# Kernel tuning notes

Measured on AMD Instinct MI355X. Metric: run time of the kernel, lower is better.

The kernel has to match this reference:

```python
import jax, jax.numpy as jnp
import numpy as np

B, N, D = 4, 1024, 512
H, Dv, Dq = 8, 64, 64
NUM_BUCKETS = 64
LN_EPS = 1e-5


def setup_inputs() -> dict:
    key = jax.random.key(0)
    ks = jax.random.split(key, 10)
    x = jax.random.normal(ks[0], (B, N, D), dtype=jnp.float32)
    ts = jnp.sort(jax.random.randint(ks[1], (B, N), 0, 1_000_000), axis=1).astype(jnp.int64)
    cm = jnp.triu(jnp.ones((N, N), dtype=bool), k=1)  # causal: mask j > i
    pm = jnp.zeros((B, N), dtype=bool)                # no padding
    uvqk = 0.02 * jax.random.normal(ks[2], (D, 2 * H * Dv + 2 * H * Dq), dtype=jnp.float32)
    lim = float(np.sqrt(6.0 / (H * Dv + D)))
    o_w = jax.random.uniform(ks[3], (H * Dv, D), minval=-lim, maxval=lim, dtype=jnp.float32)
    o_b = jnp.zeros((D,), dtype=jnp.float32)
    ln_x_w = jnp.ones((D,), jnp.float32); ln_x_b = jnp.zeros((D,), jnp.float32)
    ln_a_w = jnp.ones((H * Dv,), jnp.float32); ln_a_b = jnp.zeros((H * Dv,), jnp.float32)
    ts_w = 0.02 * jax.random.normal(ks[4], (NUM_BUCKETS + 1,), dtype=jnp.float32)
    pos_w = 0.02 * jax.random.normal(ks[5], (2 * N - 1,), dtype=jnp.float32)
    return {"x": x, "ts": ts, "cm": cm, "pm": pm, "uvqk": uvqk, "o_w": o_w, "o_b": o_b,
            "ln_x_w": ln_x_w, "ln_x_b": ln_x_b, "ln_a_w": ln_a_w, "ln_a_b": ln_a_b,
            "ts_w": ts_w, "pos_w": pos_w}


def _layernorm(x, w, b):
    m = jnp.mean(x, axis=-1, keepdims=True)
    v = jnp.mean(jnp.square(x - m), axis=-1, keepdims=True)
    return (x - m) / jnp.sqrt(v + LN_EPS) * w + b


def _rel_bias(ts, ts_w, pos_w):
    # positional part: pb[i, j] = pos_w[j - i + N - 1], shape [N, N]
    idx = jnp.arange(N)
    pb = pos_w[idx[None, :] - idx[:, None] + N - 1]
    # bucketed time part
    ext = jnp.concatenate([ts, ts[:, N - 1:N]], axis=1)           # [B, N+1]
    diff = ext[:, 1:, None] - ext[:, None, :-1]                   # [B, N, N]
    logd = jnp.log(jnp.maximum(jnp.abs(diff), 1).astype(jnp.float32))
    bk = jnp.clip((logd / 0.301).astype(jnp.int32), 0, NUM_BUCKETS)
    return pb[None] + ts_w[bk]                                    # [B, N, N]


def reference(x, ts, cm, pm, uvqk, o_w, o_b, ln_x_w, ln_x_b, ln_a_w, ln_a_b, ts_w, pos_w):
    nx = _layernorm(x, ln_x_w, ln_x_b)                            # [B, N, D]
    out = jax.nn.silu(jnp.einsum('bnd,de->bne', nx, uvqk))        # [B, N, 2HDv+2HDq]
    u, v, q, k = jnp.split(out, [H * Dv, 2 * H * Dv, 2 * H * Dv + H * Dq], axis=-1)
    q = q.reshape(B, N, H, Dq)
    k = k.reshape(B, N, H, Dq)
    v = v.reshape(B, N, H, Dv)
    qk = jnp.einsum('bihd,bjhd->bhij', q, k) + _rel_bias(ts, ts_w, pos_w)[:, None]
    qk = jax.nn.silu(qk) / N
    qk = jnp.where(cm[None, None], 0.0, qk)          # causal mask
    qk = jnp.where(pm[:, None, None, :], 0.0, qk)    # padding mask on keys
    ao = jnp.einsum('bhij,bjhd->bihd', qk, v).reshape(B, N, H * Dv)
    ao = _layernorm(ao, ln_a_w, ln_a_b)
    u = u.reshape(B, N, H * Dv)
    y = (u * ao) @ o_w + o_b + x
    return jnp.where(pm[:, :, None], 0.0, y)
```

## Files before the change

kernel.cpp:

```cpp
#include <hip/hip_runtime.h>
#include <hip/hip_bf16.h>


typedef __attribute__((ext_vector_type(8))) short short8;
typedef __attribute__((ext_vector_type(4))) short bf4;
typedef __attribute__((ext_vector_type(4))) float floatx4;

#define MFMA_BF16 __builtin_amdgcn_mfma_f32_16x16x32_bf16

static __device__ __forceinline__ short f2bf(float f) {
  unsigned u = __builtin_bit_cast(unsigned, f);
  u = (u + 0x7fffu + ((u >> 16) & 1u)) >> 16;
  return (short)u;
}
static __device__ __forceinline__ unsigned pk_bf16(float a, float b) {
  __hip_bfloat162 h = __float22bfloat162_rn(float2{a, b});
  unsigned u;
  __builtin_memcpy(&u, &h, 4);
  return u;
}
static __device__ __forceinline__ short lo16(unsigned u) { return (short)(u & 0xffffu); }
static __device__ __forceinline__ short hi16(unsigned u) { return (short)(u >> 16); }
static __device__ __forceinline__ float bf2f(short s) {
  unsigned u = ((unsigned)(unsigned short)s) << 16;
  return __builtin_bit_cast(float, u);
}
static __device__ __forceinline__ float silu_f(float x) {
  return x / (1.f + __expf(-x));
}
static __device__ __forceinline__ void gl_lds16(const void* g, void* l) {
  __builtin_amdgcn_global_load_lds(
      (const __attribute__((address_space(1))) unsigned int*)g,
      (__attribute__((address_space(3))) unsigned int*)l, 16, 0, 0);
}

__global__ __launch_bounds__(256) void prep_kernel(
    const float* __restrict__ x, const int* __restrict__ ts,
    const float* __restrict__ uvqk, const float* __restrict__ o_w,
    const float* __restrict__ ln_x_w, const float* __restrict__ ln_x_b,
    const float* __restrict__ ts_w, const float* __restrict__ pos_w,
    short* __restrict__ nx, short* __restrict__ uvqk_t,
    short* __restrict__ o_wt, short* __restrict__ bias) {
  __shared__ float tile[32][33];
  const int id = blockIdx.x;
  const int t = threadIdx.x;
  if (id < 4096) {
    const int b = id >> 10, i = id & 1023;
    int ie = i + 1; if (ie > 1023) ie = 1023;
    const int tse = ts[(b << 10) + ie];
    const int j0 = t * 4;
    int4 tj = *(const int4*)&ts[(b << 10) + j0];
    const int* tjp = (const int*)&tj;
    float ov[4];
#pragma unroll
    for (int e = 0; e < 4; ++e) {
      int dt = tse - tjp[e];
      float ad = fabsf((float)dt);
      if (ad < 1.f) ad = 1.f;
      int bkt = (int)(__logf(ad) * (1.f / 0.301f));
      if (bkt > 64) bkt = 64;
      ov[e] = pos_w[j0 + e - i + 1023] + ts_w[bkt];
    }
    uint2 o2 = {pk_bf16(ov[0], ov[1]), pk_bf16(ov[2], ov[3])};
    *(uint2*)&bias[((size_t)id << 10) + j0] = o2;
  } else if (id < 5120) {
    const int lane = t & 63;
    const int row = ((id - 4096) << 2) + (t >> 6);
    const int c0 = lane * 8;
    const float* xr = x + (size_t)row * 512;
    float v[8];
    *(float4*)&v[0] = *(const float4*)(xr + c0);
    *(float4*)&v[4] = *(const float4*)(xr + c0 + 4);
    float s = 0.f, sq = 0.f;
#pragma unroll
    for (int e = 0; e < 8; ++e) { s += v[e]; sq += v[e] * v[e]; }
#pragma unroll
    for (int off = 32; off > 0; off >>= 1) {
      s += __shfl_xor(s, off);
      sq += __shfl_xor(sq, off);
    }
    float m = s * (1.f / 512.f);
    float var = sq * (1.f / 512.f) - m * m;
    float rinv = rsqrtf(var + 1e-5f);
    float wv[8], bv[8];
    *(float4*)&wv[0] = *(const float4*)(ln_x_w + c0);
    *(float4*)&wv[4] = *(const float4*)(ln_x_w + c0 + 4);
    *(float4*)&bv[0] = *(const float4*)(ln_x_b + c0);
    *(float4*)&bv[4] = *(const float4*)(ln_x_b + c0 + 4);
    float o[8];
#pragma unroll
    for (int e = 0; e < 8; ++e) o[e] = (v[e] - m) * rinv * wv[e] + bv[e];
    uint4 o4 = {pk_bf16(o[0], o[1]), pk_bf16(o[2], o[3]),
                pk_bf16(o[4], o[5]), pk_bf16(o[6], o[7])};
    *(uint4*)(nx + (size_t)row * 512 + c0) = o4;
  } else {
    const float* src; short* dst; int R, C, bc, br;
    if (id < 6144) {
      int idm = id - 5120;
      src = uvqk; dst = uvqk_t; R = 512; C = 2048;
      bc = (idm & 63) * 32; br = (idm >> 6) * 32;
    } else {
      int idm = id - 6144;
      src = o_w; dst = o_wt; R = 512; C = 512;
      bc = (idm & 15) * 32; br = (idm >> 4) * 32;
    }
    const int c = t & 31, r0 = t >> 5;
#pragma unroll
    for (int p = 0; p < 4; ++p) {
      int r = r0 + p * 8;
      tile[r][c] = src[(size_t)(br + r) * C + bc + c];
    }
    __syncthreads();
#pragma unroll
    for (int p = 0; p < 4; ++p) {
      int r = r0 + p * 8;
      dst[(size_t)(bc + r) * R + br + c] = f2bf(tile[c][r]);
    }
  }
}

__global__ __launch_bounds__(256) void gemm1_kernel(
    const short* __restrict__ A, const short* __restrict__ Bt,
    short* __restrict__ u_buf, short* __restrict__ vt_buf,
    short* __restrict__ q_buf, short* __restrict__ k_buf) {
  __shared__ __align__(16) short As[2][128 * 32];
  __shared__ __align__(16) short Bs[2][64 * 32];
  const int t = threadIdx.x;
  const int lane = t & 63, w = t >> 6;
  const int quad = lane >> 4, l15 = lane & 15;
  const int m0 = blockIdx.x * 128, n0 = blockIdx.y * 64;
  const int wm = (w & 1) * 64, wn = (w >> 1) * 32;
  const int lr = lane >> 2, lc = (lane & 3) * 8;
  floatx4 acc[4][2];
#pragma unroll
  for (int i = 0; i < 4; ++i)
#pragma unroll
    for (int j = 0; j < 2; ++j) acc[i][j] = (floatx4){0.f, 0.f, 0.f, 0.f};

  for (int k0 = 0; k0 < 512; k0 += 64) {
    __syncthreads();
#pragma unroll
    for (int c = 0; c < 2; ++c) {
#pragma unroll
      for (int p = 0; p < 2; ++p) {
        int ra = w * 32 + p * 16;
        gl_lds16(&A[(size_t)(m0 + ra + lr) * 512 + k0 + c * 32 + lc], &As[c][ra * 32]);
      }
      int rb = w * 16;
      gl_lds16(&Bt[(size_t)(n0 + rb + lr) * 512 + k0 + c * 32 + lc], &Bs[c][rb * 32]);
    }
    __syncthreads();
#pragma unroll
    for (int c = 0; c < 2; ++c) {
      short8 af[4], bfr[2];
#pragma unroll
      for (int mi = 0; mi < 4; ++mi) af[mi] = *(const short8*)&As[c][(wm + mi * 16 + l15) * 32 + quad * 8];
#pragma unroll
      for (int ni = 0; ni < 2; ++ni) bfr[ni] = *(const short8*)&Bs[c][(wn + ni * 16 + l15) * 32 + quad * 8];
#pragma unroll
      for (int mi = 0; mi < 4; ++mi)
#pragma unroll
        for (int ni = 0; ni < 2; ++ni)
          acc[mi][ni] = MFMA_BF16(af[mi], bfr[ni], acc[mi][ni], 0, 0, 0);
    }
  }
  const int seg = n0 >> 9, cbase = n0 & 511;
  if (seg == 0) {
#pragma unroll
    for (int mi = 0; mi < 4; ++mi)
#pragma unroll
      for (int ni = 0; ni < 2; ++ni) {
        int row0 = m0 + wm + mi * 16 + quad * 4;
        int c = cbase + wn + ni * 16 + l15;
        float v0 = silu_f(acc[mi][ni][0]), v1 = silu_f(acc[mi][ni][1]);
        float v2 = silu_f(acc[mi][ni][2]), v3 = silu_f(acc[mi][ni][3]);
        unsigned pa = pk_bf16(v0, v1), pb = pk_bf16(v2, v3);
        u_buf[(size_t)row0 * 512 + c] = lo16(pa);
        u_buf[(size_t)(row0 + 1) * 512 + c] = hi16(pa);
        u_buf[(size_t)(row0 + 2) * 512 + c] = lo16(pb);
        u_buf[(size_t)(row0 + 3) * 512 + c] = hi16(pb);
      }
  } else if (seg == 1) {
#pragma unroll
    for (int mi = 0; mi < 4; ++mi)
#pragma unroll
      for (int ni = 0; ni < 2; ++ni) {
        int c = cbase + wn + ni * 16 + l15;
        int h = c >> 6, d = c & 63;
        int row0 = m0 + wm + mi * 16 + quad * 4;
        int b_ = row0 >> 10, nb = row0 & 1023;
        float v0 = silu_f(acc[mi][ni][0]) * (1.f / 1024.f);
        float v1 = silu_f(acc[mi][ni][1]) * (1.f / 1024.f);
        float v2 = silu_f(acc[mi][ni][2]) * (1.f / 1024.f);
        float v3 = silu_f(acc[mi][ni][3]) * (1.f / 1024.f);
        uint2 sv = {pk_bf16(v0, v1), pk_bf16(v2, v3)};
        *(uint2*)&vt_buf[(((size_t)(b_ * 8 + h) * 64 + d) << 10) + nb] = sv;
      }
  } else {
    short* dst = (seg == 2) ? q_buf : k_buf;
#pragma unroll
    for (int mi = 0; mi < 4; ++mi)
#pragma unroll
      for (int ni = 0; ni < 2; ++ni) {
        int row0 = m0 + wm + mi * 16 + quad * 4;
        int c = cbase + wn + ni * 16 + l15;
        int b_ = row0 >> 10, nb = row0 & 1023;
        size_t base = ((((size_t)(b_ * 8 + (c >> 6))) << 10) + nb) * 64 + (c & 63);
        float v0 = silu_f(acc[mi][ni][0]), v1 = silu_f(acc[mi][ni][1]);
        float v2 = silu_f(acc[mi][ni][2]), v3 = silu_f(acc[mi][ni][3]);
        unsigned pa = pk_bf16(v0, v1), pb = pk_bf16(v2, v3);
        dst[base] = lo16(pa);
        dst[base + 64] = hi16(pa);
        dst[base + 128] = lo16(pb);
        dst[base + 192] = hi16(pb);
      }
  }
}

__global__ __launch_bounds__(256, 4) void attn_kernel(
    const short* __restrict__ q_buf, const short* __restrict__ k_buf,
    const short* __restrict__ vt_buf, const short* __restrict__ bias_buf,
    short* __restrict__ ao_part) {
  __shared__ __align__(16) short k_s[64][72];
  __shared__ __align__(16) short vt_s[64][72];
  __shared__ __align__(16) short p_s[64][72];

  const int t = threadIdx.x;
  const int lane = t & 63, w = t >> 6;
  const int quad = lane >> 4, l15 = lane & 15;
  const int bh = blockIdx.x, pair = blockIdx.y, jh = blockIdx.z;
  const int b = bh >> 3, h = bh & 7;
  const short* qh = q_buf + (size_t)bh * 65536;
  const short* kh = k_buf + (size_t)bh * 65536;
  const short* vth = vt_buf + (size_t)bh * 65536;
  const int sr = t >> 2, sc = (t & 3) * 16;
  const int it1 = 15 - pair;
  const int i0a = pair * 64, i0b = it1 * 64;

  const short* qra = &qh[(size_t)(i0a + w * 16 + l15) * 64 + quad * 8];
  const short* qrb = &qh[(size_t)(i0b + w * 16 + l15) * 64 + quad * 8];
  short8 aqa0 = *(const short8*)qra, aqa1 = *(const short8*)(qra + 32);
  short8 aqb0 = *(const short8*)qrb, aqb1 = *(const short8*)(qrb + 32);

  floatx4 aoa[4], aob[4];
#pragma unroll
  for (int ni = 0; ni < 4; ++ni) {
    aoa[ni] = (floatx4){0.f, 0.f, 0.f, 0.f};
    aob[ni] = (floatx4){0.f, 0.f, 0.f, 0.f};
  }

  float4 kr0, kr1, vr0, vr1;
  {
    int j0 = jh * 64;
    kr0 = *(const float4*)&kh[(size_t)(j0 + sr) * 64 + sc];
    kr1 = *(const float4*)&kh[(size_t)(j0 + sr) * 64 + sc + 8];
    vr0 = *(const float4*)&vth[(size_t)sr * 1024 + j0 + sc];
    vr1 = *(const float4*)&vth[(size_t)sr * 1024 + j0 + sc + 8];
  }

  for (int jt = jh; jt <= it1; jt += 4) {
    const int j0 = jt * 64;
    __syncthreads();
    *(float4*)&k_s[sr][sc] = kr0;
    *(float4*)&k_s[sr][sc + 8] = kr1;
    *(float4*)&vt_s[sr][sc] = vr0;
    *(float4*)&vt_s[sr][sc + 8] = vr1;
    {
      int jn = (jt + 4 <= it1) ? jt + 4 : jt;
      int jn0 = jn * 64;
      kr0 = *(const float4*)&kh[(size_t)(jn0 + sr) * 64 + sc];
      kr1 = *(const float4*)&kh[(size_t)(jn0 + sr) * 64 + sc + 8];
      vr0 = *(const float4*)&vth[(size_t)sr * 1024 + jn0 + sc];
      vr1 = *(const float4*)&vth[(size_t)sr * 1024 + jn0 + sc + 8];
    }
    __syncthreads();

#pragma unroll
    for (int unit = 0; unit < 2; ++unit) {
      if (unit == 1 && jt > pair) break;
      const int i0 = unit ? i0a : i0b;
      const bool diag = (jt == (unit ? pair : it1));
      const short8 aq0 = unit ? aqa0 : aqb0;
      const short8 aq1 = unit ? aqa1 : aqb1;
      floatx4* ao = unit ? aoa : aob;
      short br[4][4];
      {
        const short* bb = &bias_buf[((size_t)(b * 1024 + i0 + w * 16 + quad * 4) << 10) + j0 + l15];
#pragma unroll
        for (int ni = 0; ni < 4; ++ni)
#pragma unroll
          for (int r2 = 0; r2 < 4; ++r2)
            br[ni][r2] = bb[((size_t)r2 << 10) + ni * 16];
      }
      floatx4 s[4];
#pragma unroll
      for (int ni = 0; ni < 4; ++ni)
#pragma unroll
        for (int r2 = 0; r2 < 4; ++r2) s[ni][r2] = bf2f(br[ni][r2]);
#pragma unroll
      for (int ni = 0; ni < 4; ++ni) {
        s[ni] = MFMA_BF16(aq0, *(const short8*)&k_s[ni * 16 + l15][quad * 8], s[ni], 0, 0, 0);
        s[ni] = MFMA_BF16(aq1, *(const short8*)&k_s[ni * 16 + l15][32 + quad * 8], s[ni], 0, 0, 0);
      }
#pragma unroll
      for (int ni = 0; ni < 4; ++ni) {
        int j_loc = ni * 16 + l15;
        float pv[4];
#pragma unroll
        for (int r2 = 0; r2 < 4; ++r2) {
          int i_loc = w * 16 + quad * 4 + r2;
          float p = silu_f(s[ni][r2]);
          pv[r2] = (diag && j_loc > i_loc) ? 0.f : p;
        }
        unsigned pa = pk_bf16(pv[0], pv[1]), pb = pk_bf16(pv[2], pv[3]);
        int ib = w * 16 + quad * 4;
        p_s[ib][j_loc] = lo16(pa);
        p_s[ib + 1][j_loc] = hi16(pa);
        p_s[ib + 2][j_loc] = lo16(pb);
        p_s[ib + 3][j_loc] = hi16(pb);
      }
      short8 ap0 = *(const short8*)&p_s[w * 16 + l15][quad * 8];
      short8 ap1 = *(const short8*)&p_s[w * 16 + l15][32 + quad * 8];
#pragma unroll
      for (int ni = 0; ni < 4; ++ni) {
        ao[ni] = MFMA_BF16(ap0, *(const short8*)&vt_s[ni * 16 + l15][quad * 8], ao[ni], 0, 0, 0);
        ao[ni] = MFMA_BF16(ap1, *(const short8*)&vt_s[ni * 16 + l15][32 + quad * 8], ao[ni], 0, 0, 0);
      }
    }
  }
  short* aod = ao_part + (size_t)jh * 2097152;
#pragma unroll
  for (int half = 0; half < 2; ++half) {
    const int i0 = half ? i0b : i0a;
    floatx4* ao = half ? aob : aoa;
#pragma unroll
    for (int ni = 0; ni < 4; ++ni) {
      int gi0 = i0 + w * 16 + quad * 4;
      int d = ni * 16 + l15;
      unsigned pa = pk_bf16(ao[ni][0], ao[ni][1]);
      unsigned pb = pk_bf16(ao[ni][2], ao[ni][3]);
      size_t base = ((size_t)(b * 1024 + gi0)) * 512 + h * 64 + d;
      aod[base] = lo16(pa);
      aod[base + 512] = hi16(pa);
      aod[base + 1024] = lo16(pb);
      aod[base + 1536] = hi16(pb);
    }
  }
}

__global__ __launch_bounds__(256) void ln_mul_kernel(
    const short* __restrict__ ao_part, const short* __restrict__ u,
    const float* __restrict__ w_, const float* __restrict__ b_,
    short* __restrict__ g) {
  const int lane = threadIdx.x & 63;
  const int row = (blockIdx.x << 2) + (threadIdx.x >> 6);
  const int c0 = lane * 8;
  short8 a0 = *(const short8*)(ao_part + (size_t)row * 512 + c0);
  short8 a1 = *(const short8*)(ao_part + 2097152 + (size_t)row * 512 + c0);
  short8 a2 = *(const short8*)(ao_part + 4194304 + (size_t)row * 512 + c0);
  short8 a3 = *(const short8*)(ao_part + 6291456 + (size_t)row * 512 + c0);
  float v[8];
#pragma unroll
  for (int e = 0; e < 8; ++e)
    v[e] = (bf2f(a0[e]) + bf2f(a1[e])) + (bf2f(a2[e]) + bf2f(a3[e]));
  float s = 0.f, sq = 0.f;
#pragma unroll
  for (int e = 0; e < 8; ++e) { s += v[e]; sq += v[e] * v[e]; }
#pragma unroll
  for (int off = 32; off > 0; off >>= 1) {
    s += __shfl_xor(s, off);
    sq += __shfl_xor(sq, off);
  }
  float m = s * (1.f / 512.f);
  float var = sq * (1.f / 512.f) - m * m;
  float rinv = rsqrtf(var + 1e-5f);
  float wv[8], bv[8];
  *(float4*)&wv[0] = *(const float4*)(w_ + c0);
  *(float4*)&wv[4] = *(const float4*)(w_ + c0 + 4);
  *(float4*)&bv[0] = *(const float4*)(b_ + c0);
  *(float4*)&bv[4] = *(const float4*)(b_ + c0 + 4);
  short8 uv = *(const short8*)(u + (size_t)row * 512 + c0);
  float o[8];
#pragma unroll
  for (int e = 0; e < 8; ++e)
    o[e] = bf2f(uv[e]) * ((v[e] - m) * rinv * wv[e] + bv[e]);
  uint4 o4 = {pk_bf16(o[0], o[1]), pk_bf16(o[2], o[3]),
              pk_bf16(o[4], o[5]), pk_bf16(o[6], o[7])};
  *(uint4*)(g + (size_t)row * 512 + c0) = o4;
}

__global__ __launch_bounds__(256) void gemm2_kernel(
    const short* __restrict__ G, const short* __restrict__ Wt,
    const float* __restrict__ o_b, const float* __restrict__ x,
    float* __restrict__ out) {
  __shared__ __align__(16) short As[2][64 * 32];
  __shared__ __align__(16) short Bs[2][64 * 32];
  const int t = threadIdx.x;
  const int lane = t & 63, w = t >> 6;
  const int quad = lane >> 4, l15 = lane & 15;
  const int m0 = blockIdx.x * 64, n0 = blockIdx.y * 64;
  const int lr = lane >> 2, lc = (lane & 3) * 8;
  floatx4 acc[4];
#pragma unroll
  for (int j = 0; j < 4; ++j) acc[j] = (floatx4){0.f, 0.f, 0.f, 0.f};

  for (int k0 = 0; k0 < 512; k0 += 64) {
    __syncthreads();
#pragma unroll
    for (int c = 0; c < 2; ++c) {
      int ra = w * 16;
      gl_lds16(&G[(size_t)(m0 + ra + lr) * 512 + k0 + c * 32 + lc], &As[c][ra * 32]);
      gl_lds16(&Wt[(size_t)(n0 + ra + lr) * 512 + k0 + c * 32 + lc], &Bs[c][ra * 32]);
    }
    __syncthreads();
#pragma unroll
    for (int c = 0; c < 2; ++c) {
      short8 af = *(const short8*)&As[c][(w * 16 + l15) * 32 + quad * 8];
#pragma unroll
      for (int ni = 0; ni < 4; ++ni) {
        short8 bfr = *(const short8*)&Bs[c][(ni * 16 + l15) * 32 + quad * 8];
        acc[ni] = MFMA_BF16(af, bfr, acc[ni], 0, 0, 0);
      }
    }
  }
#pragma unroll
  for (int ni = 0; ni < 4; ++ni)
#pragma unroll
    for (int r = 0; r < 4; ++r) {
      int row = m0 + w * 16 + quad * 4 + r;
      int c = n0 + ni * 16 + l15;
      out[(size_t)row * 512 + c] = acc[ni][r] + o_b[c] + x[(size_t)row * 512 + c];
    }
}

extern "C" void kernel_launch(void* const* d_in, const int* in_sizes, int n_in,
                              void* d_out, int out_size, void* d_ws, size_t ws_size,
                              hipStream_t stream) {
  const float* x = (const float*)d_in[0];
  const int* ts = (const int*)d_in[1];
  const float* uvqk = (const float*)d_in[4];
  const float* o_w = (const float*)d_in[5];
  const float* o_b = (const float*)d_in[6];
  const float* ln_x_w = (const float*)d_in[7];
  const float* ln_x_b = (const float*)d_in[8];
  const float* ln_a_w = (const float*)d_in[9];
  const float* ln_a_b = (const float*)d_in[10];
  const float* ts_w = (const float*)d_in[11];
  const float* pos_w = (const float*)d_in[12];
  float* out = (float*)d_out;

  char* ws = (char*)d_ws;
  short* nx = (short*)(ws + 0);
  short* uvqk_t = (short*)(ws + 4194304);
  short* o_wt = (short*)(ws + 6291456);
  short* u_buf = (short*)(ws + 6815744);
  short* q_buf = (short*)(ws + 11010048);
  short* k_buf = (short*)(ws + 15204352);
  short* vt_buf = (short*)(ws + 19398656);
  short* bias_buf = (short*)(ws + 23592960);
  short* ao_part = (short*)(ws + 31981568);
  short* g_buf = nx;

  hipLaunchKernelGGL(prep_kernel, dim3(6400), dim3(256), 0, stream,
                     x, ts, uvqk, o_w, ln_x_w, ln_x_b, ts_w, pos_w,
                     nx, uvqk_t, o_wt, bias_buf);
  hipLaunchKernelGGL(gemm1_kernel, dim3(32, 32), dim3(256), 0, stream, nx, uvqk_t, u_buf, vt_buf, q_buf, k_buf);
  hipLaunchKernelGGL(attn_kernel, dim3(32, 8, 4), dim3(256), 0, stream, q_buf, k_buf, vt_buf, bias_buf, ao_part);
  hipLaunchKernelGGL(ln_mul_kernel, dim3(1024), dim3(256), 0, stream, ao_part, u_buf, ln_a_w, ln_a_b, g_buf);
  hipLaunchKernelGGL(gemm2_kernel, dim3(64, 8), dim3(256), 0, stream, g_buf, o_wt, o_b, x, out);
}
```

Measured before the change: 141.0 us.

## Fuse five pipeline kernels into one cooperative persistent kernel with grid syncs

Replaces the five separate launches (prep, gemm1, attention, layernorm-mul, gemm2) with a single cooperative kernel of 512 blocks that loops over work items per phase and separates phases with grid.sync(). The aim is to remove per-launch overhead and inter-kernel gaps. The cost is that each phase is now limited to 512 resident blocks processing 1024 sub-tiles, plus grid-wide barriers. Load balance in the causal attention phase may also suffer. The old multi-kernel path remains as a fallback if the cooperative launch fails.

```diff
diff --git a/kernel.cpp b/kernel.cpp
--- a/kernel.cpp
+++ b/kernel.cpp
@@ -1,9 +1,11 @@
 #include <hip/hip_runtime.h>
 #include <hip/hip_bf16.h>
+#include <hip/hip_cooperative_groups.h>
+
+namespace cg = cooperative_groups;
 
 
 typedef __attribute__((ext_vector_type(8))) short short8;
-typedef __attribute__((ext_vector_type(4))) short bf4;
 typedef __attribute__((ext_vector_type(4))) float floatx4;
 
 #define MFMA_BF16 __builtin_amdgcn_mfma_f32_16x16x32_bf16
@@ -32,6 +34,412 @@
   __builtin_amdgcn_global_load_lds(
       (const __attribute__((address_space(1))) unsigned int*)g,
       (__attribute__((address_space(3))) unsigned int*)l, 16, 0, 0);
+}
+
+__global__ __launch_bounds__(256, 2) void mega_kernel(
+    const float* __restrict__ x, const int* __restrict__ ts,
+    const float* __restrict__ uvqk, const float* __restrict__ o_w,
+    const float* __restrict__ o_b, const float* __restrict__ ln_x_w,
+    const float* __restrict__ ln_x_b, const float* __restrict__ ln_a_w,
+    const float* __restrict__ ln_a_b, const float* __restrict__ ts_w,
+    const float* __restrict__ pos_w,
+    short* __restrict__ nx, short* __restrict__ uvqk_t,
+    short* __restrict__ o_wt, short* __restrict__ u_buf,
+    short* __restrict__ q_buf, short* __restrict__ k_buf,
+    short* __restrict__ vt_buf, short* __restrict__ bias_buf,
+    short* __restrict__ ao_part, short* __restrict__ g_buf,
+    float* __restrict__ out) {
+  __shared__ __align__(16) char smem[27648];
+  cg::grid_group grid = cg::this_grid();
+
+  const int gid = blockIdx.x;
+  const int t = threadIdx.x;
+  const int lane = t & 63, w = t >> 6;
+  const int quad = lane >> 4, l15 = lane & 15;
+
+  for (int sub = gid; sub < 1024; sub += 512) {
+#pragma unroll
+    for (int r = 0; r < 4; ++r) {
+      const int id = sub * 4 + r;
+      const int b = id >> 10, i = id & 1023;
+      int ie = i + 1; if (ie > 1023) ie = 1023;
+      const int tse = ts[(b << 10) + ie];
+      const int j0 = t * 4;
+      int4 tj = *(const int4*)&ts[(b << 10) + j0];
+      const int* tjp = (const int*)&tj;
+      float ov[4];
+#pragma unroll
+      for (int e = 0; e < 4; ++e) {
+        int dt = tse - tjp[e];
+        float ad = fabsf((float)dt);
+        if (ad < 1.f) ad = 1.f;
+        int bkt = (int)(__logf(ad) * (1.f / 0.301f));
+        if (bkt > 64) bkt = 64;
+        ov[e] = pos_w[j0 + e - i + 1023] + ts_w[bkt];
+      }
+      uint2 o2 = {pk_bf16(ov[0], ov[1]), pk_bf16(ov[2], ov[3])};
+      *(uint2*)&bias_buf[((size_t)id << 10) + j0] = o2;
+    }
+    {
+      const int row = (sub << 2) + w;
+      const int c0 = lane * 8;
+      const float* xr = x + (size_t)row * 512;
+      float v[8];
+      *(float4*)&v[0] = *(const float4*)(xr + c0);
+      *(float4*)&v[4] = *(const float4*)(xr + c0 + 4);
+      float s = 0.f, sq = 0.f;
+#pragma unroll
+      for (int e = 0; e < 8; ++e) { s += v[e]; sq += v[e] * v[e]; }
+#pragma unroll
+      for (int off = 32; off > 0; off >>= 1) {
+        s += __shfl_xor(s, off);
+        sq += __shfl_xor(sq, off);
+      }
+      float m = s * (1.f / 512.f);
+      float var = sq * (1.f / 512.f) - m * m;
+      float rinv = rsqrtf(var + 1e-5f);
+      float wv[8], bv[8];
+      *(float4*)&wv[0] = *(const float4*)(ln_x_w + c0);
+      *(float4*)&wv[4] = *(const float4*)(ln_x_w + c0 + 4);
+      *(float4*)&bv[0] = *(const float4*)(ln_x_b + c0);
+      *(float4*)&bv[4] = *(const float4*)(ln_x_b + c0 + 4);
+      float o[8];
+#pragma unroll
+      for (int e = 0; e < 8; ++e) o[e] = (v[e] - m) * rinv * wv[e] + bv[e];
+      uint4 o4 = {pk_bf16(o[0], o[1]), pk_bf16(o[2], o[3]),
+                  pk_bf16(o[4], o[5]), pk_bf16(o[6], o[7])};
+      *(uint4*)(nx + (size_t)row * 512 + c0) = o4;
+    }
+    float (*tile)[33] = (float(*)[33])smem;
+    {
+      __syncthreads();
+      const int bc = (sub & 63) * 32, br = (sub >> 6) * 32;
+      const int c = t & 31, r0 = t >> 5;
+#pragma unroll
+      for (int p = 0; p < 4; ++p) {
+        int r = r0 + p * 8;
+        tile[r][c] = uvqk[(size_t)(br + r) * 2048 + bc + c];
+      }
+      __syncthreads();
+#pragma unroll
+      for (int p = 0; p < 4; ++p) {
+        int r = r0 + p * 8;
+        uvqk_t[(size_t)(bc + r) * 512 + br + c] = f2bf(tile[c][r]);
+      }
+    }
+    if (sub < 256) {
+      __syncthreads();
+      const int bc = (sub & 15) * 32, br = (sub >> 4) * 32;
+      const int c = t & 31, r0 = t >> 5;
+#pragma unroll
+      for (int p = 0; p < 4; ++p) {
+        int r = r0 + p * 8;
+        tile[r][c] = o_w[(size_t)(br + r) * 512 + bc + c];
+      }
+      __syncthreads();
+#pragma unroll
+      for (int p = 0; p < 4; ++p) {
+        int r = r0 + p * 8;
+        o_wt[(size_t)(bc + r) * 512 + br + c] = f2bf(tile[c][r]);
+      }
+    }
+  }
+  grid.sync();
+
+  for (int sub = gid; sub < 1024; sub += 512) {
+    short (*As)[128 * 32] = (short(*)[128 * 32])smem;
+    short (*Bs)[64 * 32] = (short(*)[64 * 32])(smem + 16384);
+    const int m0 = (sub & 31) * 128, n0 = (sub >> 5) * 64;
+    const int wm = (w & 1) * 64, wn = (w >> 1) * 32;
+    const int lr = lane >> 2, lc = (lane & 3) * 8;
+    floatx4 acc[4][2];
+#pragma unroll
+    for (int i = 0; i < 4; ++i)
+#pragma unroll
+      for (int j = 0; j < 2; ++j) acc[i][j] = (floatx4){0.f, 0.f, 0.f, 0.f};
+
+    for (int k0 = 0; k0 < 512; k0 += 64) {
+      __syncthreads();
+#pragma unroll
+      for (int c = 0; c < 2; ++c) {
+#pragma unroll
+        for (int p = 0; p < 2; ++p) {
+          int ra = w * 32 + p * 16;
+          gl_lds16(&nx[(size_t)(m0 + ra + lr) * 512 + k0 + c * 32 + lc], &As[c][ra * 32]);
+        }
+        int rb = w * 16;
+        gl_lds16(&uvqk_t[(size_t)(n0 + rb + lr) * 512 + k0 + c * 32 + lc], &Bs[c][rb * 32]);
+      }
+      __syncthreads();
+#pragma unroll
+      for (int c = 0; c < 2; ++c) {
+        short8 af[4], bfr[2];
+#pragma unroll
+        for (int mi = 0; mi < 4; ++mi) af[mi] = *(const short8*)&As[c][(wm + mi * 16 + l15) * 32 + quad * 8];
+#pragma unroll
+        for (int ni = 0; ni < 2; ++ni) bfr[ni] = *(const short8*)&Bs[c][(wn + ni * 16 + l15) * 32 + quad * 8];
+#pragma unroll
+        for (int mi = 0; mi < 4; ++mi)
+#pragma unroll
+          for (int ni = 0; ni < 2; ++ni)
+            acc[mi][ni] = MFMA_BF16(af[mi], bfr[ni], acc[mi][ni], 0, 0, 0);
+      }
+    }
+    const int seg = n0 >> 9, cbase = n0 & 511;
+    if (seg == 0) {
+#pragma unroll
+      for (int mi = 0; mi < 4; ++mi)
+#pragma unroll
+        for (int ni = 0; ni < 2; ++ni) {
+          int row0 = m0 + wm + mi * 16 + quad * 4;
+          int c = cbase + wn + ni * 16 + l15;
+          float v0 = silu_f(acc[mi][ni][0]), v1 = silu_f(acc[mi][ni][1]);
+          float v2 = silu_f(acc[mi][ni][2]), v3 = silu_f(acc[mi][ni][3]);
+          unsigned pa = pk_bf16(v0, v1), pb = pk_bf16(v2, v3);
+          u_buf[(size_t)row0 * 512 + c] = lo16(pa);
+          u_buf[(size_t)(row0 + 1) * 512 + c] = hi16(pa);
+          u_buf[(size_t)(row0 + 2) * 512 + c] = lo16(pb);
+          u_buf[(size_t)(row0 + 3) * 512 + c] = hi16(pb);
+        }
+    } else if (seg == 1) {
+#pragma unroll
+      for (int mi = 0; mi < 4; ++mi)
+#pragma unroll
+        for (int ni = 0; ni < 2; ++ni) {
+          int c = cbase + wn + ni * 16 + l15;
+          int h = c >> 6, d = c & 63;
+          int row0 = m0 + wm + mi * 16 + quad * 4;
+          int b_ = row0 >> 10, nb = row0 & 1023;
+          float v0 = silu_f(acc[mi][ni][0]) * (1.f / 1024.f);
+          float v1 = silu_f(acc[mi][ni][1]) * (1.f / 1024.f);
+          float v2 = silu_f(acc[mi][ni][2]) * (1.f / 1024.f);
+          float v3 = silu_f(acc[mi][ni][3]) * (1.f / 1024.f);
+          uint2 sv = {pk_bf16(v0, v1), pk_bf16(v2, v3)};
+          *(uint2*)&vt_buf[(((size_t)(b_ * 8 + h) * 64 + d) << 10) + nb] = sv;
+        }
+    } else {
+      short* dst = (seg == 2) ? q_buf : k_buf;
+#pragma unroll
+      for (int mi = 0; mi < 4; ++mi)
+#pragma unroll
+        for (int ni = 0; ni < 2; ++ni) {
+          int row0 = m0 + wm + mi * 16 + quad * 4;
+          int c = cbase + wn + ni * 16 + l15;
+          int b_ = row0 >> 10, nb = row0 & 1023;
+          size_t base = ((((size_t)(b_ * 8 + (c >> 6))) << 10) + nb) * 64 + (c & 63);
+          float v0 = silu_f(acc[mi][ni][0]), v1 = silu_f(acc[mi][ni][1]);
+          float v2 = silu_f(acc[mi][ni][2]), v3 = silu_f(acc[mi][ni][3]);
+          unsigned pa = pk_bf16(v0, v1), pb = pk_bf16(v2, v3);
+          dst[base] = lo16(pa);
+          dst[base + 64] = hi16(pa);
+          dst[base + 128] = lo16(pb);
+          dst[base + 192] = hi16(pb);
+        }
+    }
+  }
+  grid.sync();
+
+  for (int sub = gid; sub < 1024; sub += 512) {
+    short (*k_s)[72] = (short(*)[72])smem;
+    short (*vt_s)[72] = (short(*)[72])(smem + 9216);
+    short (*p_s)[72] = (short(*)[72])(smem + 18432);
+    const int bh = sub & 31, pair = (sub >> 5) & 7, jh = sub >> 8;
+    const int b = bh >> 3, h = bh & 7;
+    const short* qh = q_buf + (size_t)bh * 65536;
+    const short* kh = k_buf + (size_t)bh * 65536;
+    const short* vth = vt_buf + (size_t)bh * 65536;
+    const int sr = t >> 2, sc = (t & 3) * 16;
+    const int it1 = 15 - pair;
+    const int i0a = pair * 64, i0b = it1 * 64;
+
+    const short* qra = &qh[(size_t)(i0a + w * 16 + l15) * 64 + quad * 8];
+    const short* qrb = &qh[(size_t)(i0b + w * 16 + l15) * 64 + quad * 8];
+    short8 aqa0 = *(const short8*)qra, aqa1 = *(const short8*)(qra + 32);
+    short8 aqb0 = *(const short8*)qrb, aqb1 = *(const short8*)(qrb + 32);
+
+    floatx4 aoa[4], aob[4];
+#pragma unroll
+    for (int ni = 0; ni < 4; ++ni) {
+      aoa[ni] = (floatx4){0.f, 0.f, 0.f, 0.f};
+      aob[ni] = (floatx4){0.f, 0.f, 0.f, 0.f};
+    }
+
+    float4 kr0, kr1, vr0, vr1;
+    {
+      int j0 = jh * 64;
+      kr0 = *(const float4*)&kh[(size_t)(j0 + sr) * 64 + sc];
+      kr1 = *(const float4*)&kh[(size_t)(j0 + sr) * 64 + sc + 8];
+      vr0 = *(const float4*)&vth[(size_t)sr * 1024 + j0 + sc];
+      vr1 = *(const float4*)&vth[(size_t)sr * 1024 + j0 + sc + 8];
+    }
+
+    for (int jt = jh; jt <= it1; jt += 4) {
+      const int j0 = jt * 64;
+      __syncthreads();
+      *(float4*)&k_s[sr][sc] = kr0;
+      *(float4*)&k_s[sr][sc + 8] = kr1;
+      *(float4*)&vt_s[sr][sc] = vr0;
+      *(float4*)&vt_s[sr][sc + 8] = vr1;
+      {
+        int jn = (jt + 4 <= it1) ? jt + 4 : jt;
+        int jn0 = jn * 64;
+        kr0 = *(const float4*)&kh[(size_t)(jn0 + sr) * 64 + sc];
+        kr1 = *(const float4*)&kh[(size_t)(jn0 + sr) * 64 + sc + 8];
+        vr0 = *(const float4*)&vth[(size_t)sr * 1024 + jn0 + sc];
+        vr1 = *(const float4*)&vth[(size_t)sr * 1024 + jn0 + sc + 8];
+      }
+      __syncthreads();
+
+#pragma unroll
+      for (int unit = 0; unit < 2; ++unit) {
+        if (unit == 1 && jt > pair) break;
+        const int i0 = unit ? i0a : i0b;
+        const bool diag = (jt == (unit ? pair : it1));
+        const short8 aq0 = unit ? aqa0 : aqb0;
+        const short8 aq1 = unit ? aqa1 : aqb1;
+        floatx4* ao = unit ? aoa : aob;
+        short br[4][4];
+        {
+          const short* bb = &bias_buf[((size_t)(b * 1024 + i0 + w * 16 + quad * 4) << 10) + j0 + l15];
+#pragma unroll
+          for (int ni = 0; ni < 4; ++ni)
+#pragma unroll
+            for (int r2 = 0; r2 < 4; ++r2)
+              br[ni][r2] = bb[((size_t)r2 << 10) + ni * 16];
+        }
+        floatx4 s[4];
+#pragma unroll
+        for (int ni = 0; ni < 4; ++ni)
+#pragma unroll
+          for (int r2 = 0; r2 < 4; ++r2) s[ni][r2] = bf2f(br[ni][r2]);
+#pragma unroll
+        for (int ni = 0; ni < 4; ++ni) {
+          s[ni] = MFMA_BF16(aq0, *(const short8*)&k_s[ni * 16 + l15][quad * 8], s[ni], 0, 0, 0);
+          s[ni] = MFMA_BF16(aq1, *(const short8*)&k_s[ni * 16 + l15][32 + quad * 8], s[ni], 0, 0, 0);
+        }
+#pragma unroll
+        for (int ni = 0; ni < 4; ++ni) {
+          int j_loc = ni * 16 + l15;
+          float pv[4];
+#pragma unroll
+          for (int r2 = 0; r2 < 4; ++r2) {
+            int i_loc = w * 16 + quad * 4 + r2;
+            float p = silu_f(s[ni][r2]);
+            pv[r2] = (diag && j_loc > i_loc) ? 0.f : p;
+          }
+          unsigned pa = pk_bf16(pv[0], pv[1]), pb = pk_bf16(pv[2], pv[3]);
+          int ib = w * 16 + quad * 4;
+          p_s[ib][j_loc] = lo16(pa);
+          p_s[ib + 1][j_loc] = hi16(pa);
+          p_s[ib + 2][j_loc] = lo16(pb);
+          p_s[ib + 3][j_loc] = hi16(pb);
+        }
+        short8 ap0 = *(const short8*)&p_s[w * 16 + l15][quad * 8];
+        short8 ap1 = *(const short8*)&p_s[w * 16 + l15][32 + quad * 8];
+#pragma unroll
+        for (int ni = 0; ni < 4; ++ni) {
+          ao[ni] = MFMA_BF16(ap0, *(const short8*)&vt_s[ni * 16 + l15][quad * 8], ao[ni], 0, 0, 0);
+          ao[ni] = MFMA_BF16(ap1, *(const short8*)&vt_s[ni * 16 + l15][32 + quad * 8], ao[ni], 0, 0, 0);
+        }
+      }
+    }
+    short* aod = ao_part + (size_t)jh * 2097152;
+#pragma unroll
+    for (int half = 0; half < 2; ++half) {
+      const int i0 = half ? i0b : i0a;
+      floatx4* ao = half ? aob : aoa;
+#pragma unroll
+      for (int ni = 0; ni < 4; ++ni) {
+        int gi0 = i0 + w * 16 + quad * 4;
+        int d = ni * 16 + l15;
+        unsigned pa = pk_bf16(ao[ni][0], ao[ni][1]);
+        unsigned pb = pk_bf16(ao[ni][2], ao[ni][3]);
+        size_t base = ((size_t)(b * 1024 + gi0)) * 512 + h * 64 + d;
+        aod[base] = lo16(pa);
+        aod[base + 512] = hi16(pa);
+        aod[base + 1024] = lo16(pb);
+        aod[base + 1536] = hi16(pb);
+      }
+    }
+  }
+  grid.sync();
+
+  for (int sub = gid; sub < 1024; sub += 512) {
+    const int row = (sub << 2) + w;
+    const int c0 = lane * 8;
+    short8 a0 = *(const short8*)(ao_part + (size_t)row * 512 + c0);
+    short8 a1 = *(const short8*)(ao_part + 2097152 + (size_t)row * 512 + c0);
+    short8 a2 = *(const short8*)(ao_part + 4194304 + (size_t)row * 512 + c0);
+    short8 a3 = *(const short8*)(ao_part + 6291456 + (size_t)row * 512 + c0);
+    float v[8];
+#pragma unroll
+    for (int e = 0; e < 8; ++e)
+      v[e] = (bf2f(a0[e]) + bf2f(a1[e])) + (bf2f(a2[e]) + bf2f(a3[e]));
+    float s = 0.f, sq = 0.f;
+#pragma unroll
+    for (int e = 0; e < 8; ++e) { s += v[e]; sq += v[e] * v[e]; }
+#pragma unroll
+    for (int off = 32; off > 0; off >>= 1) {
+      s += __shfl_xor(s, off);
+      sq += __shfl_xor(sq, off);
+    }
+    float m = s * (1.f / 512.f);
+    float var = sq * (1.f / 512.f) - m * m;
+    float rinv = rsqrtf(var + 1e-5f);
+    float wv[8], bv[8];
+    *(float4*)&wv[0] = *(const float4*)(ln_a_w + c0);
+    *(float4*)&wv[4] = *(const float4*)(ln_a_w + c0 + 4);
+    *(float4*)&bv[0] = *(const float4*)(ln_a_b + c0);
+    *(float4*)&bv[4] = *(const float4*)(ln_a_b + c0 + 4);
+    short8 uv = *(const short8*)(u_buf + (size_t)row * 512 + c0);
+    float o[8];
+#pragma unroll
+    for (int e = 0; e < 8; ++e)
+      o[e] = bf2f(uv[e]) * ((v[e] - m) * rinv * wv[e] + bv[e]);
+    uint4 o4 = {pk_bf16(o[0], o[1]), pk_bf16(o[2], o[3]),
+                pk_bf16(o[4], o[5]), pk_bf16(o[6], o[7])};
+    *(uint4*)(g_buf + (size_t)row * 512 + c0) = o4;
+  }
+  grid.sync();
+
+  for (int sub = gid; sub < 1024; sub += 512) {
+    short (*As)[32 * 32] = (short(*)[32 * 32])smem;
+    short (*Bs)[64 * 32] = (short(*)[64 * 32])(smem + 4096);
+    const int m0 = (sub >> 3) * 32, n0 = (sub & 7) * 64;
+    const int lr = lane >> 2, lc = (lane & 3) * 8;
+    const int rw = (w & 1) * 16, cw = (w >> 1) * 32;
+    floatx4 acc[2];
+#pragma unroll
+    for (int j = 0; j < 2; ++j) acc[j] = (floatx4){0.f, 0.f, 0.f, 0.f};
+
+    for (int k0 = 0; k0 < 512; k0 += 64) {
+      __syncthreads();
+#pragma unroll
+      for (int c = 0; c < 2; ++c) {
+        if (w < 2)
+          gl_lds16(&g_buf[(size_t)(m0 + w * 16 + lr) * 512 + k0 + c * 32 + lc], &As[c][w * 16 * 32]);
+        gl_lds16(&o_wt[(size_t)(n0 + w * 16 + lr) * 512 + k0 + c * 32 + lc], &Bs[c][w * 16 * 32]);
+      }
+      __syncthreads();
+#pragma unroll
+      for (int c = 0; c < 2; ++c) {
+        short8 af = *(const short8*)&As[c][(rw + l15) * 32 + quad * 8];
+#pragma unroll
+        for (int ni = 0; ni < 2; ++ni) {
+          short8 bfr = *(const short8*)&Bs[c][(cw + ni * 16 + l15) * 32 + quad * 8];
+          acc[ni] = MFMA_BF16(af, bfr, acc[ni], 0, 0, 0);
+        }
+      }
+    }
+#pragma unroll
+    for (int ni = 0; ni < 2; ++ni)
+#pragma unroll
+      for (int r = 0; r < 4; ++r) {
+        int row = m0 + rw + quad * 4 + r;
+        int c = n0 + cw + ni * 16 + l15;
+        out[(size_t)row * 512 + c] = acc[ni][r] + o_b[c] + x[(size_t)row * 512 + c];
+      }
+  }
 }
 
 __global__ __launch_bounds__(256) void prep_kernel(
@@ -461,11 +869,23 @@
   short* ao_part = (short*)(ws + 31981568);
   short* g_buf = nx;
 
-  hipLaunchKernelGGL(prep_kernel, dim3(6400), dim3(256), 0, stream,
-                     x, ts, uvqk, o_w, ln_x_w, ln_x_b, ts_w, pos_w,
-                     nx, uvqk_t, o_wt, bias_buf);
-  hipLaunchKernelGGL(gemm1_kernel, dim3(32, 32), dim3(256), 0, stream, nx, uvqk_t, u_buf, vt_buf, q_buf, k_buf);
-  hipLaunchKernelGGL(attn_kernel, dim3(32, 8, 4), dim3(256), 0, stream, q_buf, k_buf, vt_buf, bias_buf, ao_part);
-  hipLaunchKernelGGL(ln_mul_kernel, dim3(1024), dim3(256), 0, stream, ao_part, u_buf, ln_a_w, ln_a_b, g_buf);
-  hipLaunchKernelGGL(gemm2_kernel, dim3(64, 8), dim3(256), 0, stream, g_buf, o_wt, o_b, x, out);
-}
+  void* args[] = {&x, &ts, &uvqk, &o_w, &o_b, &ln_x_w, &ln_x_b, &ln_a_w,
+                  &ln_a_b, &ts_w, &pos_w, &nx, &uvqk_t, &o_wt, &u_buf,
+                  &q_buf, &k_buf, &vt_buf, &bias_buf, &ao_part, &g_buf, &out};
+  hipError_t err = hipLaunchCooperativeKernel((const void*)mega_kernel,
+                                              dim3(512), dim3(256), args, 0, stream);
+  if (err != hipSuccess) {
+    (void)hipGetLastError();
+    hipLaunchKernelGGL(prep_kernel, dim3(6400), dim3(256), 0, stream,
+                       x, ts, uvqk, o_w, ln_x_w, ln_x_b, ts_w, pos_w,
+                       nx, uvqk_t, o_wt, bias_buf);
+    hipLaunchKernelGGL(gemm1_kernel, dim3(32, 32), dim3(256), 0, stream,
+                       nx, uvqk_t, u_buf, vt_buf, q_buf, k_buf);
+    hipLaunchKernelGGL(attn_kernel, dim3(32, 8, 4), dim3(256), 0, stream,
+                       q_buf, k_buf, vt_buf, bias_buf, ao_part);
+    hipLaunchKernelGGL(ln_mul_kernel, dim3(1024), dim3(256), 0, stream,
+                       ao_part, u_buf, ln_a_w, ln_a_b, g_buf);
+    hipLaunchKernelGGL(gemm2_kernel, dim3(64, 8), dim3(256), 0, stream,
+                       g_buf, o_wt, o_b, x, out);
+  }
+}
```

Result: slower. 420.1 us (+197.9%).
